# Optimization experiments

Hardware: AMD Instinct MI355X
Metric: run time of the kernel (lower is better)

## Reference

```python
import jax, jax.numpy as jnp
import numpy as np

N_HEAD = 16
R = 4  # reciprocal rank

def setup_inputs() -> dict:
    key = jax.random.key(0)
    ks = jax.random.split(key, 8)
    B, T, C = 2, 2048, 1024
    H = N_HEAD
    D = C // H
    D_std = D - R
    x = jax.random.normal(ks[0], (B, T, C), dtype=jnp.float32)
    W_attn = jax.random.normal(ks[1], (3 * C, C), dtype=jnp.float32) * (1.0 / np.sqrt(C))
    W_proj = jax.random.normal(ks[2], (C, C), dtype=jnp.float32) * (1.0 / np.sqrt(C))
    w_std = jnp.full((H,), D_std / D, dtype=jnp.float32)
    w_rec = jnp.full((H,), R / D, dtype=jnp.float32)
    skip_std = jnp.float32(2.0)
    skip_low = jnp.float32(-3.0)
    rwr_alpha = jnp.full((H,), 0.05, dtype=jnp.float32)
    return {"x": x, "W_attn": W_attn, "W_proj": W_proj, "w_std": w_std,
            "w_rec": w_rec, "skip_std": skip_std, "skip_low": skip_low,
            "rwr_alpha": rwr_alpha}

def reference(x, W_attn, W_proj, w_std, w_rec, skip_std, skip_low, rwr_alpha):
    B, T, C = x.shape
    H = N_HEAD
    D = C // H
    D_std = D - R
    # fused QKV projection: [Qf | Kf | V]
    fused = jnp.einsum('btc,fc->btf', x, W_attn)
    qf, kf, v = jnp.split(fused, 3, axis=-1)
    Qf = qf.reshape(B, T, H, D).transpose(0, 2, 1, 3)  # (B,H,T,D)
    Kf = kf.reshape(B, T, H, D).transpose(0, 2, 1, 3)
    V = v.reshape(B, T, H, D).transpose(0, 2, 1, 3)
    # dynamic per-head gate scaling folded into Qf/Kf
    g_std = jnp.sqrt(jnp.clip(w_std * jax.nn.sigmoid(skip_std), 1e-8))  # (H,)
    g_rec = jnp.sqrt(jnp.clip(w_rec * jax.nn.sigmoid(skip_low), 1e-8))  # (H,)
    scale = jnp.concatenate([
        jnp.broadcast_to(g_std[:, None], (H, D_std)),
        jnp.broadcast_to(g_rec[:, None], (H, R)),
    ], axis=-1)  # (H, D)
    scale = scale[None, :, None, :]  # (1,H,1,D)
    Qf = Qf * scale
    Kf = Kf * scale
    # causal SDPA (scale = 1/sqrt(head_dim), dropout=0)
    scores = jnp.einsum('bhqd,bhkd->bhqk', Qf, Kf) / jnp.sqrt(jnp.float32(D))
    causal = jnp.tril(jnp.ones((T, T), dtype=bool))
    scores = jnp.where(causal[None, None], scores, jnp.float32(-1e30))
    attn = jax.nn.softmax(scores, axis=-1)
    y = jnp.einsum('bhqk,bhkd->bhqd', attn, V)
    # self-restart mix: out = (1-alpha)*attn_out + alpha*V, alpha in [0, 0.5]
    alpha = jnp.clip(rwr_alpha, 0.0, 0.5)[None, :, None, None]
    y = (1.0 - alpha) * y + alpha * V
    y = y.transpose(0, 2, 1, 3).reshape(B, T, C)
    return jnp.einsum('btc,oc->bto', y, W_proj)
```

## Files before the change

kernel.cpp:

```cpp
#include <hip/hip_runtime.h>
#include <hip/hip_bf16.h>
#include <math.h>
#include <stdint.h>

#define B_    2
#define T_    2048
#define C_    1024
#define H_    16
#define D_    64
#define R_    4
#define DSTD  60
#define F_    3072
#define BT_   (B_ * T_)

#define LOG2E 1.44269504088896340736f

typedef __bf16 bf16x8 __attribute__((ext_vector_type(8)));
typedef __bf16 bf16x4 __attribute__((ext_vector_type(4)));
typedef float  f32x4  __attribute__((ext_vector_type(4)));
typedef float  f32x16 __attribute__((ext_vector_type(16)));

__device__ __forceinline__ int swz(int row, int blk) {
    return blk ^ ((row >> 1) & 7);
}

__device__ __forceinline__ void gload_lds16(const void* g, void* l) {
    __builtin_amdgcn_global_load_lds(
        (const __attribute__((address_space(1))) uint32_t*)g,
        (__attribute__((address_space(3))) uint32_t*)l, 16, 0, 0);
}

__device__ __forceinline__ uint32_t pack2(float lo, float hi) {
    union { __bf16 h[2]; uint32_t u; } t;
    t.h[0] = (__bf16)lo; t.h[1] = (__bf16)hi;
    return t.u;
}

__device__ __forceinline__ void plswap(uint32_t& a, uint32_t& b) {
    asm volatile("v_permlane32_swap_b32 %0, %1" : "+v"(a), "+v"(b));
}

__global__ __launch_bounds__(256) void cast3_kernel(
    const float* __restrict__ a, int na4,
    const float* __restrict__ b, int nb4,
    const float* __restrict__ c, int nc4,
    __bf16* __restrict__ oa, __bf16* __restrict__ ob, __bf16* __restrict__ oc)
{
    int i = blockIdx.x * 256 + threadIdx.x;
    const float* s; __bf16* d; int j = i;
    if (j < na4) { s = a; d = oa; }
    else {
        j -= na4;
        if (j < nb4) { s = b; d = ob; }
        else {
            j -= nb4;
            if (j >= nc4) return;
            s = c; d = oc;
        }
    }
    float4 v = ((const float4*)s)[j];
    bf16x4 o;
    o[0] = (__bf16)v.x; o[1] = (__bf16)v.y;
    o[2] = (__bf16)v.z; o[3] = (__bf16)v.w;
    ((bf16x4*)d)[j] = o;
}

__global__ __launch_bounds__(256) void gemm_qkv_kernel(
    const __bf16* __restrict__ A,
    const __bf16* __restrict__ Bw,
    const float* __restrict__ w_std, const float* __restrict__ w_rec,
    const float* __restrict__ skip_std, const float* __restrict__ skip_low,
    __bf16* __restrict__ Q, __bf16* __restrict__ K, __bf16* __restrict__ V)
{
    __shared__ __bf16 As[128 * 32];
    __shared__ __bf16 Bs[128 * 32];

    const int tid  = threadIdx.x;
    const int row0 = blockIdx.x * 128;
    const int col0 = blockIdx.y * 128;

    const int w    = tid >> 6;
    const int lane = tid & 63;
    const int quad = lane >> 4;
    const int lt   = lane & 15;
    const int wm   = w >> 1;
    const int wn   = w & 1;

    const int lrow = tid >> 2;
    const int lcol = (tid & 3) * 8;

    f32x4 acc[4][4];
#pragma unroll
    for (int i = 0; i < 4; ++i)
#pragma unroll
        for (int j = 0; j < 4; ++j)
#pragma unroll
            for (int r = 0; r < 4; ++r) acc[i][j][r] = 0.f;

    for (int kt = 0; kt < C_ / 32; ++kt) {
        const int k0 = kt * 32;
        __syncthreads();
#pragma unroll
        for (int rr = 0; rr < 2; ++rr) {
            gload_lds16(A  + (size_t)(row0 + rr * 64 + lrow) * C_ + k0 + lcol,
                        As + rr * 2048 + tid * 8);
            gload_lds16(Bw + (size_t)(col0 + rr * 64 + lrow) * C_ + k0 + lcol,
                        Bs + rr * 2048 + tid * 8);
        }
        __syncthreads();

        bf16x8 af[4], bf[4];
#pragma unroll
        for (int i = 0; i < 4; ++i)
            af[i] = *(const bf16x8*)&As[(wm * 64 + i * 16 + lt) * 32 + quad * 8];
#pragma unroll
        for (int j = 0; j < 4; ++j)
            bf[j] = *(const bf16x8*)&Bs[(wn * 64 + j * 16 + lt) * 32 + quad * 8];
#pragma unroll
        for (int i = 0; i < 4; ++i)
#pragma unroll
            for (int j = 0; j < 4; ++j)
                acc[i][j] = __builtin_amdgcn_mfma_f32_16x16x32_bf16(af[i], bf[j], acc[i][j], 0, 0, 0);
    }

    const int colbase = col0 + wn * 64;
    const int which   = colbase >> 10;
    const int h       = (colbase & (C_ - 1)) >> 6;

    const float ss = 1.f / (1.f + __expf(-skip_std[0]));
    const float sl = 1.f / (1.f + __expf(-skip_low[0]));
    const float gs = sqrtf(fmaxf(w_std[h] * ss, 1e-8f));
    const float gr = sqrtf(fmaxf(w_rec[h] * sl, 1e-8f));

    __bf16* dstM = (which == 0) ? Q : (which == 1) ? K : V;

#pragma unroll
    for (int i = 0; i < 4; ++i) {
#pragma unroll
        for (int r = 0; r < 4; ++r) {
            const int row = row0 + wm * 64 + i * 16 + quad * 4 + r;
            const int b = row >> 11;
            const int t = row & (T_ - 1);
            __bf16* dp = dstM + (((size_t)b * H_ + h) * T_ + t) * D_;
#pragma unroll
            for (int j = 0; j < 4; ++j) {
                const int d = j * 16 + lt;
                float val = acc[i][j][r];
                if (which == 0)      val *= ((d < DSTD) ? gs : gr) * (0.125f * LOG2E);
                else if (which == 1) val *= (d < DSTD) ? gs : gr;
                dp[d] = (__bf16)val;
            }
        }
    }
}

__global__ __launch_bounds__(256) void gemm_out_kernel(
    const __bf16* __restrict__ A,
    const __bf16* __restrict__ Bw,
    float* __restrict__ out)
{
    __shared__ __bf16 As[128 * 32];
    __shared__ __bf16 Bs[128 * 32];

    const int tid  = threadIdx.x;
    const int row0 = blockIdx.x * 128;
    const int col0 = blockIdx.y * 128;

    const int w    = tid >> 6;
    const int lane = tid & 63;
    const int quad = lane >> 4;
    const int lt   = lane & 15;
    const int wm   = w >> 1;
    const int wn   = w & 1;

    const int lrow = tid >> 2;
    const int lcol = (tid & 3) * 8;

    f32x4 acc[4][4];
#pragma unroll
    for (int i = 0; i < 4; ++i)
#pragma unroll
        for (int j = 0; j < 4; ++j)
#pragma unroll
            for (int r = 0; r < 4; ++r) acc[i][j][r] = 0.f;

    for (int kt = 0; kt < C_ / 32; ++kt) {
        const int k0 = kt * 32;
        __syncthreads();
#pragma unroll
        for (int rr = 0; rr < 2; ++rr) {
            gload_lds16(A  + (size_t)(row0 + rr * 64 + lrow) * C_ + k0 + lcol,
                        As + rr * 2048 + tid * 8);
            gload_lds16(Bw + (size_t)(col0 + rr * 64 + lrow) * C_ + k0 + lcol,
                        Bs + rr * 2048 + tid * 8);
        }
        __syncthreads();

        bf16x8 af[4], bf[4];
#pragma unroll
        for (int i = 0; i < 4; ++i)
            af[i] = *(const bf16x8*)&As[(wm * 64 + i * 16 + lt) * 32 + quad * 8];
#pragma unroll
        for (int j = 0; j < 4; ++j)
            bf[j] = *(const bf16x8*)&Bs[(wn * 64 + j * 16 + lt) * 32 + quad * 8];
#pragma unroll
        for (int i = 0; i < 4; ++i)
#pragma unroll
            for (int j = 0; j < 4; ++j)
                acc[i][j] = __builtin_amdgcn_mfma_f32_16x16x32_bf16(af[i], bf[j], acc[i][j], 0, 0, 0);
    }

#pragma unroll
    for (int i = 0; i < 4; ++i)
#pragma unroll
        for (int r = 0; r < 4; ++r) {
            const int row = row0 + wm * 64 + i * 16 + quad * 4 + r;
            float* op = out + (size_t)row * C_ + col0 + wn * 64 + lt;
#pragma unroll
            for (int j = 0; j < 4; ++j)
                op[j * 16] = acc[i][j][r];
        }
}

__global__ __launch_bounds__(128) void attn_kernel(
    const __bf16* __restrict__ Q, const __bf16* __restrict__ K,
    const __bf16* __restrict__ V, const float* __restrict__ rwr_alpha,
    __bf16* __restrict__ Y)
{
    __shared__ __align__(16) __bf16 Ks[2][64][64];
    __shared__ __align__(16) __bf16 Vt[2][64][64];

    const int tid = threadIdx.x;
    const int bh  = blockIdx.x & 31;
    const int g   = blockIdx.x >> 5;
    const int qt  = (g < 8) ? (31 - g) : (g < 16) ? (g - 8)
                  : (g < 24) ? (39 - g) : (g - 16);
    const int h   = bh & (H_ - 1);
    const int b   = bh >> 4;

    const __bf16* Qb = Q + (((size_t)b * H_ + h) * T_) * D_;
    const __bf16* Kb = K + (((size_t)b * H_ + h) * T_) * D_;
    const __bf16* Vb = V + (((size_t)b * H_ + h) * T_) * D_;

    const int w    = tid >> 6;
    const int lane = tid & 63;
    const int lq   = lane & 31;
    const int hi   = lane >> 5;

    const int krb = tid >> 3;
    const int kcb = tid & 7;

    const int kp = (tid >> 3) * 4;
    const int dc = (tid & 7) * 8;
    const int vblk = kp >> 3, voff = kp & 7;

    const __bf16* qrow = Qb + (size_t)(qt * 64 + w * 32 + lq) * D_;
    bf16x8 qf[4];
#pragma unroll
    for (int kk = 0; kk < 4; ++kk)
        qf[kk] = *(const bf16x8*)(qrow + kk * 16 + hi * 8);

    bf16x8 ones;
#pragma unroll
    for (int u = 0; u < 8; ++u) ones[u] = (__bf16)1.0f;

#pragma unroll
    for (int cc = 0; cc < 4; ++cc) {
        const int kr = cc * 16 + krb;
        const int kc = kcb ^ ((kr >> 1) & 7);
        gload_lds16(Kb + (size_t)kr * 64 + kc * 8,
                    &Ks[0][0][0] + cc * 1024 + tid * 8);
    }
    {
        const __bf16* vs = Vb + (size_t)kp * 64 + dc;
        bf16x8 v0 = *(const bf16x8*)(vs);
        bf16x8 v1 = *(const bf16x8*)(vs + 64);
        bf16x8 v2 = *(const bf16x8*)(vs + 128);
        bf16x8 v3 = *(const bf16x8*)(vs + 192);
#pragma unroll
        for (int u = 0; u < 8; ++u) {
            const int row = dc + u;
            bf16x4 t; t[0] = v0[u]; t[1] = v1[u]; t[2] = v2[u]; t[3] = v3[u];
            *(bf16x4*)&Vt[0][row][swz(row, vblk) * 8 + voff] = t;
        }
    }
    __syncthreads();

    f32x16 oacc[2], lacc;
#pragma unroll
    for (int r = 0; r < 16; ++r) { oacc[0][r] = 0.f; oacc[1][r] = 0.f; lacc[r] = 0.f; }

    for (int kt = 0; kt <= qt; ++kt) {
        const int cur = kt & 1;
        const int nxt = cur ^ 1;
        const bool pre = (kt < qt);

        bf16x8 v0, v1, v2, v3;
        if (pre) {
            const size_t toff = (size_t)(kt + 1) * 4096;
#pragma unroll
            for (int cc = 0; cc < 4; ++cc) {
                const int kr = cc * 16 + krb;
                const int kc = kcb ^ ((kr >> 1) & 7);
                gload_lds16(Kb + toff + (size_t)kr * 64 + kc * 8,
                            &Ks[nxt][0][0] + cc * 1024 + tid * 8);
            }
            const __bf16* vs = Vb + toff + (size_t)kp * 64 + dc;
            v0 = *(const bf16x8*)(vs);
            v1 = *(const bf16x8*)(vs + 64);
            v2 = *(const bf16x8*)(vs + 128);
            v3 = *(const bf16x8*)(vs + 192);
        }

#pragma unroll
        for (int kb = 0; kb < 2; ++kb) {
            f32x16 sacc;
#pragma unroll
            for (int r = 0; r < 16; ++r) sacc[r] = 0.f;
            const int arow = kb * 32 + lq;
#pragma unroll
            for (int kk = 0; kk < 4; ++kk) {
                bf16x8 ak = *(const bf16x8*)&Ks[cur][arow][swz(arow, kk * 2 + hi) * 8];
                sacc = __builtin_amdgcn_mfma_f32_32x32x16_bf16(ak, qf[kk], sacc, 0, 0, 0);
            }

            if (kt == qt) {
                const int ql = w * 32 + lq;
#pragma unroll
                for (int r = 0; r < 16; ++r) {
                    const int key = kb * 32 + (r & 3) + ((r >> 2) << 3) + hi * 4;
                    if (key > ql) sacc[r] = -1e30f;
                }
            }

#pragma unroll
            for (int c = 0; c < 2; ++c) {
                const int rb = 8 * c;
                float p0 = __builtin_amdgcn_exp2f(sacc[rb + 0]);
                float p1 = __builtin_amdgcn_exp2f(sacc[rb + 1]);
                float p2 = __builtin_amdgcn_exp2f(sacc[rb + 2]);
                float p3 = __builtin_amdgcn_exp2f(sacc[rb + 3]);
                float p4 = __builtin_amdgcn_exp2f(sacc[rb + 4]);
                float p5 = __builtin_amdgcn_exp2f(sacc[rb + 5]);
                float p6 = __builtin_amdgcn_exp2f(sacc[rb + 6]);
                float p7 = __builtin_amdgcn_exp2f(sacc[rb + 7]);

                uint32_t w0 = pack2(p0, p1);
                uint32_t w2 = pack2(p4, p5);
                plswap(w0, w2);
                uint32_t w1 = pack2(p2, p3);
                uint32_t w3 = pack2(p6, p7);
                plswap(w1, w3);

                union { uint32_t u[4]; bf16x8 v; } pf;
                pf.u[0] = w0; pf.u[1] = w1; pf.u[2] = w2; pf.u[3] = w3;

                lacc = __builtin_amdgcn_mfma_f32_32x32x16_bf16(pf.v, ones, lacc, 0, 0, 0);

                const int kk2 = kb * 2 + c;
#pragma unroll
                for (int db = 0; db < 2; ++db) {
                    const int drow = db * 32 + lq;
                    bf16x8 bv = *(const bf16x8*)&Vt[cur][drow][swz(drow, kk2 * 2 + hi) * 8];
                    oacc[db] = __builtin_amdgcn_mfma_f32_32x32x16_bf16(pf.v, bv, oacc[db], 0, 0, 0);
                }
            }
        }

        {
            float lm = lacc[0];
#pragma unroll
            for (int r = 1; r < 16; ++r) lm = fmaxf(lm, lacc[r]);
            if (__ballot(lm > 1.0e12f)) {
                const float sc = 1.0f / 4294967296.0f;
#pragma unroll
                for (int r = 0; r < 16; ++r) {
                    lacc[r] *= sc; oacc[0][r] *= sc; oacc[1][r] *= sc;
                }
            }
        }

        if (pre) {
#pragma unroll
            for (int u = 0; u < 8; ++u) {
                const int row = dc + u;
                bf16x4 t; t[0] = v0[u]; t[1] = v1[u]; t[2] = v2[u]; t[3] = v3[u];
                *(bf16x4*)&Vt[nxt][row][swz(row, vblk) * 8 + voff] = t;
            }
        }
        __syncthreads();
    }

    const float a = fminf(fmaxf(rwr_alpha[h], 0.f), 0.5f);
#pragma unroll
    for (int r = 0; r < 16; ++r) {
        const float inv = 1.f / lacc[r];
        const int qg = qt * 64 + w * 32 + (r & 3) + ((r >> 2) << 3) + hi * 4;
        const __bf16* vp = Vb + (size_t)qg * D_;
        __bf16* yp = Y + ((size_t)(b * T_ + qg)) * C_ + h * D_;
#pragma unroll
        for (int db = 0; db < 2; ++db) {
            const int d = db * 32 + lq;
            yp[d] = (__bf16)((1.f - a) * oacc[db][r] * inv + a * (float)vp[d]);
        }
    }
}

extern "C" void kernel_launch(void* const* d_in, const int* in_sizes, int n_in,
                              void* d_out, int out_size, void* d_ws, size_t ws_size,
                              hipStream_t stream) {
    const float* x        = (const float*)d_in[0];
    const float* W_attn   = (const float*)d_in[1];
    const float* W_proj   = (const float*)d_in[2];
    const float* w_std    = (const float*)d_in[3];
    const float* w_rec    = (const float*)d_in[4];
    const float* skip_std = (const float*)d_in[5];
    const float* skip_low = (const float*)d_in[6];
    const float* rwr      = (const float*)d_in[7];
    float* out = (float*)d_out;

    const size_t nX  = (size_t)BT_ * C_;
    const size_t nWa = (size_t)F_ * C_;
    const size_t nWp = (size_t)C_ * C_;
    const size_t per = (size_t)B_ * H_ * T_ * D_;

    __bf16* xb  = (__bf16*)d_ws;
    __bf16* Wab = xb  + nX;
    __bf16* Wpb = Wab + nWa;
    __bf16* Qb  = Wpb + nWp;
    __bf16* Kb  = Qb  + per;
    __bf16* Vb  = Kb  + per;
    __bf16* Yb  = Vb  + per;

    const int na4 = nX / 4, nb4 = nWa / 4, nc4 = nWp / 4;
    cast3_kernel<<<dim3((na4 + nb4 + nc4 + 255) / 256), 256, 0, stream>>>(
        x, na4, W_attn, nb4, W_proj, nc4, xb, Wab, Wpb);

    gemm_qkv_kernel<<<dim3(BT_ / 128, F_ / 128), 256, 0, stream>>>(
        xb, Wab, w_std, w_rec, skip_std, skip_low, Qb, Kb, Vb);
    attn_kernel<<<dim3(32 * (T_ / 64)), 128, 0, stream>>>(Qb, Kb, Vb, rwr, Yb);
    gemm_out_kernel<<<dim3(BT_ / 128, C_ / 128), 256, 0, stream>>>(Yb, Wpb, out);
}
```

Baseline: 196.8 us.

## Split attention key tiles across two wave groups with LDS reduction

The attention block grows from 128 to 256 threads. Each pair of waves now handles one half of every 64-key tile instead of both halves. Partial row sums and output accumulators from the second key-group are written to shared memory and added by the first group before the epilogue. The goal is more waves per block, which shortens each wave's serial MFMA/exp chain and spreads K/V tile loading over more threads. The cost is an extra LDS reduction, a sync at the end, and half the waves sitting idle during the epilogue.

```diff
diff --git a/kernel.cpp b/kernel.cpp
--- a/kernel.cpp
+++ b/kernel.cpp
@@ -22,6 +22,12 @@
 
 __device__ __forceinline__ int swz(int row, int blk) {
     return blk ^ ((row >> 1) & 7);
+}
+
+__device__ __forceinline__ void st_pair(__bf16* p, __bf16 a, __bf16 b) {
+    union { __bf16 h[2]; uint32_t u; } t;
+    t.h[0] = a; t.h[1] = b;
+    *(uint32_t*)p = t.u;
 }
 
 __device__ __forceinline__ void gload_lds16(const void* g, void* l) {
@@ -222,13 +228,12 @@
         }
 }
 
-__global__ __launch_bounds__(128) void attn_kernel(
+__global__ __launch_bounds__(256) void attn_kernel(
     const __bf16* __restrict__ Q, const __bf16* __restrict__ K,
     const __bf16* __restrict__ V, const float* __restrict__ rwr_alpha,
     __bf16* __restrict__ Y)
 {
-    __shared__ __align__(16) __bf16 Ks[2][64][64];
-    __shared__ __align__(16) __bf16 Vt[2][64][64];
+    __shared__ __align__(16) __bf16 KsV[2][2][64][64];
 
     const int tid = threadIdx.x;
     const int bh  = blockIdx.x & 31;
@@ -246,15 +251,17 @@
     const int lane = tid & 63;
     const int lq   = lane & 31;
     const int hi   = lane >> 5;
+    const int qh   = w & 1;
+    const int kg   = w >> 1;
 
     const int krb = tid >> 3;
     const int kcb = tid & 7;
 
-    const int kp = (tid >> 3) * 4;
+    const int kp = (tid >> 3) * 2;
     const int dc = (tid & 7) * 8;
     const int vblk = kp >> 3, voff = kp & 7;
 
-    const __bf16* qrow = Qb + (size_t)(qt * 64 + w * 32 + lq) * D_;
+    const __bf16* qrow = Qb + (size_t)(qt * 64 + qh * 32 + lq) * D_;
     bf16x8 qf[4];
 #pragma unroll
     for (int kk = 0; kk < 4; ++kk)
@@ -265,23 +272,20 @@
     for (int u = 0; u < 8; ++u) ones[u] = (__bf16)1.0f;
 
 #pragma unroll
-    for (int cc = 0; cc < 4; ++cc) {
-        const int kr = cc * 16 + krb;
+    for (int cc = 0; cc < 2; ++cc) {
+        const int kr = cc * 32 + krb;
         const int kc = kcb ^ ((kr >> 1) & 7);
         gload_lds16(Kb + (size_t)kr * 64 + kc * 8,
-                    &Ks[0][0][0] + cc * 1024 + tid * 8);
+                    &KsV[0][0][0][0] + cc * 2048 + tid * 8);
     }
     {
         const __bf16* vs = Vb + (size_t)kp * 64 + dc;
-        bf16x8 v0 = *(const bf16x8*)(vs);
-        bf16x8 v1 = *(const bf16x8*)(vs + 64);
-        bf16x8 v2 = *(const bf16x8*)(vs + 128);
-        bf16x8 v3 = *(const bf16x8*)(vs + 192);
+        bf16x8 v1 = *(const bf16x8*)(vs);
+        bf16x8 v2 = *(const bf16x8*)(vs + 64);
 #pragma unroll
         for (int u = 0; u < 8; ++u) {
             const int row = dc + u;
-            bf16x4 t; t[0] = v0[u]; t[1] = v1[u]; t[2] = v2[u]; t[3] = v3[u];
-            *(bf16x4*)&Vt[0][row][swz(row, vblk) * 8 + voff] = t;
+            st_pair(&KsV[1][0][row][swz(row, vblk) * 8 + voff], v1[u], v2[u]);
         }
     }
     __syncthreads();
@@ -295,75 +299,70 @@
         const int nxt = cur ^ 1;
         const bool pre = (kt < qt);
 
-        bf16x8 v0, v1, v2, v3;
+        bf16x8 v1, v2;
         if (pre) {
             const size_t toff = (size_t)(kt + 1) * 4096;
 #pragma unroll
-            for (int cc = 0; cc < 4; ++cc) {
-                const int kr = cc * 16 + krb;
+            for (int cc = 0; cc < 2; ++cc) {
+                const int kr = cc * 32 + krb;
                 const int kc = kcb ^ ((kr >> 1) & 7);
                 gload_lds16(Kb + toff + (size_t)kr * 64 + kc * 8,
-                            &Ks[nxt][0][0] + cc * 1024 + tid * 8);
+                            &KsV[0][nxt][0][0] + cc * 2048 + tid * 8);
             }
             const __bf16* vs = Vb + toff + (size_t)kp * 64 + dc;
-            v0 = *(const bf16x8*)(vs);
-            v1 = *(const bf16x8*)(vs + 64);
-            v2 = *(const bf16x8*)(vs + 128);
-            v3 = *(const bf16x8*)(vs + 192);
-        }
-
-#pragma unroll
-        for (int kb = 0; kb < 2; ++kb) {
-            f32x16 sacc;
-#pragma unroll
-            for (int r = 0; r < 16; ++r) sacc[r] = 0.f;
-            const int arow = kb * 32 + lq;
-#pragma unroll
-            for (int kk = 0; kk < 4; ++kk) {
-                bf16x8 ak = *(const bf16x8*)&Ks[cur][arow][swz(arow, kk * 2 + hi) * 8];
-                sacc = __builtin_amdgcn_mfma_f32_32x32x16_bf16(ak, qf[kk], sacc, 0, 0, 0);
-            }
-
-            if (kt == qt) {
-                const int ql = w * 32 + lq;
-#pragma unroll
-                for (int r = 0; r < 16; ++r) {
-                    const int key = kb * 32 + (r & 3) + ((r >> 2) << 3) + hi * 4;
-                    if (key > ql) sacc[r] = -1e30f;
-                }
-            }
-
-#pragma unroll
-            for (int c = 0; c < 2; ++c) {
-                const int rb = 8 * c;
-                float p0 = __builtin_amdgcn_exp2f(sacc[rb + 0]);
-                float p1 = __builtin_amdgcn_exp2f(sacc[rb + 1]);
-                float p2 = __builtin_amdgcn_exp2f(sacc[rb + 2]);
-                float p3 = __builtin_amdgcn_exp2f(sacc[rb + 3]);
-                float p4 = __builtin_amdgcn_exp2f(sacc[rb + 4]);
-                float p5 = __builtin_amdgcn_exp2f(sacc[rb + 5]);
-                float p6 = __builtin_amdgcn_exp2f(sacc[rb + 6]);
-                float p7 = __builtin_amdgcn_exp2f(sacc[rb + 7]);
-
-                uint32_t w0 = pack2(p0, p1);
-                uint32_t w2 = pack2(p4, p5);
-                plswap(w0, w2);
-                uint32_t w1 = pack2(p2, p3);
-                uint32_t w3 = pack2(p6, p7);
-                plswap(w1, w3);
-
-                union { uint32_t u[4]; bf16x8 v; } pf;
-                pf.u[0] = w0; pf.u[1] = w1; pf.u[2] = w2; pf.u[3] = w3;
-
-                lacc = __builtin_amdgcn_mfma_f32_32x32x16_bf16(pf.v, ones, lacc, 0, 0, 0);
-
-                const int kk2 = kb * 2 + c;
-#pragma unroll
-                for (int db = 0; db < 2; ++db) {
-                    const int drow = db * 32 + lq;
-                    bf16x8 bv = *(const bf16x8*)&Vt[cur][drow][swz(drow, kk2 * 2 + hi) * 8];
-                    oacc[db] = __builtin_amdgcn_mfma_f32_32x32x16_bf16(pf.v, bv, oacc[db], 0, 0, 0);
-                }
+            v1 = *(const bf16x8*)(vs);
+            v2 = *(const bf16x8*)(vs + 64);
+        }
+
+        f32x16 sacc;
+#pragma unroll
+        for (int r = 0; r < 16; ++r) sacc[r] = 0.f;
+        const int arow = kg * 32 + lq;
+#pragma unroll
+        for (int kk = 0; kk < 4; ++kk) {
+            bf16x8 ak = *(const bf16x8*)&KsV[0][cur][arow][swz(arow, kk * 2 + hi) * 8];
+            sacc = __builtin_amdgcn_mfma_f32_32x32x16_bf16(ak, qf[kk], sacc, 0, 0, 0);
+        }
+
+        if (kt == qt) {
+            const int ql = qh * 32 + lq;
+#pragma unroll
+            for (int r = 0; r < 16; ++r) {
+                const int key = kg * 32 + (r & 3) + ((r >> 2) << 3) + hi * 4;
+                if (key > ql) sacc[r] = -1e30f;
+            }
+        }
+
+#pragma unroll
+        for (int c = 0; c < 2; ++c) {
+            const int rb = 8 * c;
+            float p0 = __builtin_amdgcn_exp2f(sacc[rb + 0]);
+            float p1 = __builtin_amdgcn_exp2f(sacc[rb + 1]);
+            float p2 = __builtin_amdgcn_exp2f(sacc[rb + 2]);
+            float p3 = __builtin_amdgcn_exp2f(sacc[rb + 3]);
+            float p4 = __builtin_amdgcn_exp2f(sacc[rb + 4]);
+            float p5 = __builtin_amdgcn_exp2f(sacc[rb + 5]);
+            float p6 = __builtin_amdgcn_exp2f(sacc[rb + 6]);
+            float p7 = __builtin_amdgcn_exp2f(sacc[rb + 7]);
+
+            uint32_t w0 = pack2(p0, p1);
+            uint32_t w2 = pack2(p4, p5);
+            plswap(w0, w2);
+            uint32_t w1 = pack2(p2, p3);
+            uint32_t w3 = pack2(p6, p7);
+            plswap(w1, w3);
+
+            union { uint32_t u[4]; bf16x8 v; } pf;
+            pf.u[0] = w0; pf.u[1] = w1; pf.u[2] = w2; pf.u[3] = w3;
+
+            lacc = __builtin_amdgcn_mfma_f32_32x32x16_bf16(pf.v, ones, lacc, 0, 0, 0);
+
+            const int kk2 = kg * 2 + c;
+#pragma unroll
+            for (int db = 0; db < 2; ++db) {
+                const int drow = db * 32 + lq;
+                bf16x8 bv = *(const bf16x8*)&KsV[1][cur][drow][swz(drow, kk2 * 2 + hi) * 8];
+                oacc[db] = __builtin_amdgcn_mfma_f32_32x32x16_bf16(pf.v, bv, oacc[db], 0, 0, 0);
             }
         }
 
@@ -384,25 +383,48 @@
 #pragma unroll
             for (int u = 0; u < 8; ++u) {
                 const int row = dc + u;
-                bf16x4 t; t[0] = v0[u]; t[1] = v1[u]; t[2] = v2[u]; t[3] = v3[u];
-                *(bf16x4*)&Vt[nxt][row][swz(row, vblk) * 8 + voff] = t;
+                st_pair(&KsV[1][nxt][row][swz(row, vblk) * 8 + voff], v1[u], v2[u]);
             }
         }
         __syncthreads();
     }
 
+    float* red = (float*)&KsV[0][0][0][0];
+    union { f32x16 v; f32x4 c[4]; } ul, u0, u1;
+    ul.v = lacc; u0.v = oacc[0]; u1.v = oacc[1];
+
+    if (kg == 1) {
+        f32x4* dst = (f32x4*)red;
+#pragma unroll
+        for (int j = 0; j < 4; ++j) {
+            dst[((j     ) * 2 + qh) * 64 + lane] = ul.c[j];
+            dst[((j +  4) * 2 + qh) * 64 + lane] = u0.c[j];
+            dst[((j +  8) * 2 + qh) * 64 + lane] = u1.c[j];
+        }
+    }
+    __syncthreads();
+    if (kg == 1) return;
+
+    {
+        const f32x4* src = (const f32x4*)red;
+#pragma unroll
+        for (int j = 0; j < 4; ++j) {
+            ul.c[j] += src[((j     ) * 2 + qh) * 64 + lane];
+            u0.c[j] += src[((j +  4) * 2 + qh) * 64 + lane];
+            u1.c[j] += src[((j +  8) * 2 + qh) * 64 + lane];
+        }
+    }
+
     const float a = fminf(fmaxf(rwr_alpha[h], 0.f), 0.5f);
 #pragma unroll
     for (int r = 0; r < 16; ++r) {
-        const float inv = 1.f / lacc[r];
-        const int qg = qt * 64 + w * 32 + (r & 3) + ((r >> 2) << 3) + hi * 4;
+        const float inv = 1.f / ul.v[r];
+        const int qg = qt * 64 + qh * 32 + (r & 3) + ((r >> 2) << 3) + hi * 4;
         const __bf16* vp = Vb + (size_t)qg * D_;
         __bf16* yp = Y + ((size_t)(b * T_ + qg)) * C_ + h * D_;
-#pragma unroll
-        for (int db = 0; db < 2; ++db) {
-            const int d = db * 32 + lq;
-            yp[d] = (__bf16)((1.f - a) * oacc[db][r] * inv + a * (float)vp[d]);
-        }
+        const float o0 = u0.v[r], o1 = u1.v[r];
+        yp[lq]      = (__bf16)((1.f - a) * o0 * inv + a * (float)vp[lq]);
+        yp[32 + lq] = (__bf16)((1.f - a) * o1 * inv + a * (float)vp[32 + lq]);
     }
 }
 
@@ -438,6 +460,6 @@
 
     gemm_qkv_kernel<<<dim3(BT_ / 128, F_ / 128), 256, 0, stream>>>(
         xb, Wab, w_std, w_rec, skip_std, skip_low, Qb, Kb, Vb);
-    attn_kernel<<<dim3(32 * (T_ / 64)), 128, 0, stream>>>(Qb, Kb, Vb, rwr, Yb);
+    attn_kernel<<<dim3(32 * (T_ / 64)), 256, 0, stream>>>(Qb, Kb, Vb, rwr, Yb);
     gemm_out_kernel<<<dim3(BT_ / 128, C_ / 128), 256, 0, stream>>>(Yb, Wpb, out);
 }
```

Result: slower. 202.6 us (+2.9%).
